# Performance work log

Measured on AMD Instinct MI355X. Metric: run time of the kernel, lower is better.

Reference implementation:

```python
import jax, jax.numpy as jnp
import numpy as np

EPS = 1e-5

def _ln(x, g, b):
    m = jnp.mean(x, axis=-1, keepdims=True)
    v = jnp.var(x, axis=-1, keepdims=True)
    return (x - m) * jax.lax.rsqrt(v + EPS) * g + b

def _gelu(x):
    return jax.nn.gelu(x, approximate=False)  # torch nn.GELU default is exact erf

def setup_inputs() -> dict:
    key = jax.random.key(0)
    B, N, D, H = 4, 1024, 128, 12
    HID = H * D
    ks = jax.random.split(key, 16)
    s = lambda k, sh, fan: jax.random.normal(k, sh, jnp.float32) * (fan ** -0.5)
    return {
        "x": jax.random.normal(ks[0], (B, N, D), jnp.float32),
        # project: LN(D) -> Linear(D,HID) -> GELU -> Linear(HID,HID)
        "ln1_g": jnp.ones((D,), jnp.float32), "ln1_b": jnp.zeros((D,), jnp.float32),
        "W1": s(ks[1], (D, HID), D), "b1": jnp.zeros((HID,), jnp.float32),
        "W2": s(ks[2], (HID, HID), HID), "b2": jnp.zeros((HID,), jnp.float32),
        # shared Attention(inc=D, outc=D)
        "aln_g": jnp.ones((D,), jnp.float32), "aln_b": jnp.zeros((D,), jnp.float32),
        "Wqkv": s(ks[3], (D, 3 * D), D), "bqkv": jnp.zeros((3 * D,), jnp.float32),
        "Wl": s(ks[4], (D, D), D), "bl": jnp.zeros((D,), jnp.float32),
        # out_proj: LN(HID) -> Linear(HID, D) -> GELU
        "lno_g": jnp.ones((HID,), jnp.float32), "lno_b": jnp.zeros((HID,), jnp.float32),
        "Wo": s(ks[5], (HID, D), HID), "bo": jnp.zeros((D,), jnp.float32),
    }

def reference(x, ln1_g, ln1_b, W1, b1, W2, b2,
              aln_g, aln_b, Wqkv, bqkv, Wl, bl,
              lno_g, lno_b, Wo, bo):
    B, N, D = x.shape
    # project (dropout is identity in eval mode)
    h = _ln(x, ln1_g, ln1_b)
    h = _gelu(h @ W1 + b1)
    h = h @ W2 + b2                      # [B, N, H*D]
    H = h.shape[-1] // D
    # chunk along last dim into H features of width D; fold heads into batch
    f = h.reshape(B, N, H, D).transpose(0, 2, 1, 3).reshape(B * H, N, D)
    # shared Attention applied to each head-chunk
    a = _ln(f, aln_g, aln_b)
    qkv = a @ Wqkv + bqkv
    q, k, v = jnp.split(qkv, 3, axis=-1)
    scores = jax.nn.softmax(jnp.einsum('bnd,bmd->bnm', q, k) * (D ** -0.5), axis=-1)
    o = jnp.einsum('bnm,bmd->bnd', scores, v)
    o = o @ Wl + bl
    o = _gelu(o + f)                     # [B*H, N, D]
    # concat heads back along last dim
    feats = o.reshape(B, H, N, D).transpose(0, 2, 1, 3).reshape(B, N, H * D)
    out = _gelu(_ln(feats, lno_g, lno_b) @ Wo + bo)
    return out
```

## Files before the change

kernel.cpp:

```cpp
#include <hip/hip_runtime.h>
#include <stdint.h>

typedef unsigned short u16;
typedef __attribute__((ext_vector_type(8))) short short8;
typedef __attribute__((ext_vector_type(4))) float floatx4;

__device__ inline float b2f(u16 u) {
  union { uint32_t i; float f; } x; x.i = ((uint32_t)u) << 16; return x.f;
}
__device__ inline u16 f2b(float f) {
  union { float f; uint32_t i; } x; x.f = f;
  uint32_t r = (x.i + 0x7FFFu + ((x.i >> 16) & 1u)) >> 16;
  return (u16)r;
}
__device__ inline float gelu_f(float v) {
  return 0.5f * v * (1.0f + erff(v * 0.70710678118654752440f));
}

#define MFMA16(a, b, c) __builtin_amdgcn_mfma_f32_16x16x32_bf16((a), (b), (c), 0, 0, 0)

__device__ __forceinline__ void gl2lds16(const u16* g, u16* l) {
  __builtin_amdgcn_global_load_lds(
      (const __attribute__((address_space(1))) uint32_t*)(uintptr_t)g,
      (__attribute__((address_space(3))) uint32_t*)(uint32_t)(uintptr_t)l,
      16, 0, 0);
}

__global__ __launch_bounds__(256)
void tpose_all_kernel(const float* __restrict__ W1, const float* __restrict__ W2,
                      const float* __restrict__ Wqkv, const float* __restrict__ Wl,
                      const float* __restrict__ Wo,
                      u16* __restrict__ w1t, u16* __restrict__ w2t,
                      u16* __restrict__ wqkvt, u16* __restrict__ wlt,
                      u16* __restrict__ wot) {
  int id = blockIdx.x;
  const float* src; u16* dst; int R, C, bx, by;
  if (id < 2304)      { src = W2;   dst = w2t;   R = 1536; C = 1536; bx = (id % 48) * 32; by = (id / 48) * 32; }
  else if (id < 2496) { id -= 2304; src = W1;   dst = w1t;   R = 128;  C = 1536; bx = (id % 48) * 32; by = (id / 48) * 32; }
  else if (id < 2688) { id -= 2496; src = Wo;   dst = wot;   R = 1536; C = 128;  bx = (id % 4) * 32;  by = (id / 4) * 32; }
  else if (id < 2736) { id -= 2688; src = Wqkv; dst = wqkvt; R = 128;  C = 384;  bx = (id % 12) * 32; by = (id / 12) * 32; }
  else                { id -= 2736; src = Wl;   dst = wlt;   R = 128;  C = 128;  bx = (id % 4) * 32;  by = (id / 4) * 32; }
  __shared__ u16 t[32][33];
  int tx = threadIdx.x & 31, ty = threadIdx.x >> 5;
  for (int i = 0; i < 32; i += 8)
    t[ty + i][tx] = f2b(src[(size_t)(by + ty + i) * C + bx + tx]);
  __syncthreads();
  for (int i = 0; i < 32; i += 8)
    dst[(size_t)(bx + ty + i) * R + by + tx] = t[tx][ty + i];
}

__global__ __launch_bounds__(256)
void vtrans_kernel(const u16* __restrict__ qkv, u16* __restrict__ vT) {
  int bh = blockIdx.y;
  int n0 = blockIdx.x * 32;
  int b = bh / 12, h = bh % 12;
  const int rs = 12 * 384;
  const u16* vp = qkv + (((size_t)b * 1024) * 12 + h) * 384 + 256;
  __shared__ u16 t[4][32][33];
  int tx = threadIdx.x & 31, ty = threadIdx.x >> 5;
  for (int dt = 0; dt < 4; dt++)
    for (int i = 0; i < 32; i += 8)
      t[dt][ty + i][tx] = vp[(size_t)(n0 + ty + i) * rs + dt * 32 + tx];
  __syncthreads();
  u16* dp = vT + (size_t)bh * 128 * 1024 + n0;
  for (int dt = 0; dt < 4; dt++)
    for (int i = 0; i < 32; i += 8)
      dp[(size_t)(dt * 32 + ty + i) * 1024 + tx] = t[dt][tx][ty + i];
}

__global__ __launch_bounds__(256)
void ln128_f32_kernel(const float* __restrict__ X, const float* __restrict__ g,
                      const float* __restrict__ bb, u16* __restrict__ Y) {
  int tid = threadIdx.x, w = tid >> 6, lane = tid & 63;
  int row = blockIdx.x * 4 + w;
  const float* xr = X + (size_t)row * 128;
  float2 xv = *(const float2*)(xr + lane * 2);
  float x0 = xv.x, x1 = xv.y;
  float s = x0 + x1, s2 = x0 * x0 + x1 * x1;
  for (int m = 1; m < 64; m <<= 1) { s += __shfl_xor(s, m, 64); s2 += __shfl_xor(s2, m, 64); }
  float mean = s * (1.0f / 128.0f);
  float var = s2 * (1.0f / 128.0f) - mean * mean;
  float rstd = 1.0f / sqrtf(var + 1e-5f);
  float2 gv = *(const float2*)(g + lane * 2);
  float2 bv = *(const float2*)(bb + lane * 2);
  float y0 = (x0 - mean) * rstd * gv.x + bv.x;
  float y1 = (x1 - mean) * rstd * gv.y + bv.y;
  *(uint32_t*)(Y + (size_t)row * 128 + lane * 2) =
      (uint32_t)f2b(y0) | ((uint32_t)f2b(y1) << 16);
}

__global__ __launch_bounds__(256)
void ln128_bf16_kernel(const u16* __restrict__ X, const float* __restrict__ g,
                       const float* __restrict__ bb, u16* __restrict__ Y) {
  int tid = threadIdx.x, w = tid >> 6, lane = tid & 63;
  int row = blockIdx.x * 4 + w;
  const u16* xr = X + (size_t)row * 128;
  uint32_t u = *(const uint32_t*)(xr + lane * 2);
  float x0 = b2f(u & 0xffff), x1 = b2f(u >> 16);
  float s = x0 + x1, s2 = x0 * x0 + x1 * x1;
  for (int m = 1; m < 64; m <<= 1) { s += __shfl_xor(s, m, 64); s2 += __shfl_xor(s2, m, 64); }
  float mean = s * (1.0f / 128.0f);
  float var = s2 * (1.0f / 128.0f) - mean * mean;
  float rstd = 1.0f / sqrtf(var + 1e-5f);
  float2 gv = *(const float2*)(g + lane * 2);
  float2 bv = *(const float2*)(bb + lane * 2);
  float y0 = (x0 - mean) * rstd * gv.x + bv.x;
  float y1 = (x1 - mean) * rstd * gv.y + bv.y;
  *(uint32_t*)(Y + (size_t)row * 128 + lane * 2) =
      (uint32_t)f2b(y0) | ((uint32_t)f2b(y1) << 16);
}

__global__ __launch_bounds__(256)
void ln1536_kernel(const u16* __restrict__ X, const float* __restrict__ g,
                   const float* __restrict__ bb, u16* __restrict__ Y) {
  int row = blockIdx.x, tid = threadIdx.x;
  const u16* xr = X + (size_t)row * 1536;
  uint32_t u0 = *(const uint32_t*)(xr + tid * 6);
  uint32_t u1 = *(const uint32_t*)(xr + tid * 6 + 2);
  uint32_t u2 = *(const uint32_t*)(xr + tid * 6 + 4);
  float v[6] = { b2f(u0 & 0xffff), b2f(u0 >> 16), b2f(u1 & 0xffff),
                 b2f(u1 >> 16),    b2f(u2 & 0xffff), b2f(u2 >> 16) };
  float s = 0.f, s2 = 0.f;
  for (int j = 0; j < 6; j++) { s += v[j]; s2 += v[j] * v[j]; }
  for (int m = 1; m < 64; m <<= 1) { s += __shfl_xor(s, m, 64); s2 += __shfl_xor(s2, m, 64); }
  __shared__ float red[8];
  int w = tid >> 6, lane = tid & 63;
  if (lane == 0) { red[w] = s; red[4 + w] = s2; }
  __syncthreads();
  s = red[0] + red[1] + red[2] + red[3];
  s2 = red[4] + red[5] + red[6] + red[7];
  float mean = s * (1.0f / 1536.0f);
  float var = s2 * (1.0f / 1536.0f) - mean * mean;
  float rstd = 1.0f / sqrtf(var + 1e-5f);
  uint32_t o[3];
  for (int p = 0; p < 3; p++) {
    int c = tid * 6 + p * 2;
    float y0 = (v[p * 2] - mean) * rstd * g[c] + bb[c];
    float y1 = (v[p * 2 + 1] - mean) * rstd * g[c + 1] + bb[c + 1];
    o[p] = (uint32_t)f2b(y0) | ((uint32_t)f2b(y1) << 16);
  }
  u16* yr = Y + (size_t)row * 1536 + tid * 6;
  *(uint32_t*)(yr) = o[0];
  *(uint32_t*)(yr + 2) = o[1];
  *(uint32_t*)(yr + 4) = o[2];
}

template <int GELU, int RES, typename OUTT>
__global__ __launch_bounds__(256)
void gemm_kernel(const u16* __restrict__ A, const u16* __restrict__ BT,
                 const float* __restrict__ bias, const u16* __restrict__ res,
                 OUTT* __restrict__ C, int M, int N, int K) {
  __shared__ __align__(16) u16 abuf[128 * 32];
  __shared__ __align__(16) u16 bbuf[128 * 32];
  int tid = threadIdx.x;
  int w = tid >> 6, lane = tid & 63, ln = lane & 15, quad = lane >> 4;
  int bm = blockIdx.x * 128, bn = blockIdx.y * 128;
  int wr = w >> 1, wc = w & 1;
  floatx4 acc[4][4] = {};
  for (int k0 = 0; k0 < K; k0 += 32) {
    __syncthreads();
    for (int rd = 0; rd < 2; rd++) {
      int c = tid + rd * 256;
      int row = c >> 2, col = (c & 3) * 8;
      gl2lds16(A + (size_t)(bm + row) * K + k0 + col, abuf + c * 8);
      gl2lds16(BT + (size_t)(bn + row) * K + k0 + col, bbuf + c * 8);
    }
    __syncthreads();
    short8 af[4], bf[4];
    for (int i = 0; i < 4; i++)
      af[i] = *(const short8*)(abuf + (wr * 64 + i * 16 + ln) * 32 + quad * 8);
    for (int j = 0; j < 4; j++)
      bf[j] = *(const short8*)(bbuf + (wc * 64 + j * 16 + ln) * 32 + quad * 8);
    for (int i = 0; i < 4; i++)
      for (int j = 0; j < 4; j++)
        acc[i][j] = MFMA16(af[i], bf[j], acc[i][j]);
  }
  for (int i = 0; i < 4; i++) {
    int row0 = bm + wr * 64 + i * 16 + quad * 4;
    for (int j = 0; j < 4; j++) {
      int col = bn + wc * 64 + j * 16 + ln;
      float bv = bias[col];
      for (int r = 0; r < 4; r++) {
        float v = acc[i][j][r] + bv;
        if (RES) v += b2f(res[(size_t)(row0 + r) * N + col]);
        if (GELU) v = gelu_f(v);
        if constexpr (sizeof(OUTT) == 2)
          C[(size_t)(row0 + r) * N + col] = f2b(v);
        else
          C[(size_t)(row0 + r) * N + col] = v;
      }
    }
  }
}

template <int GELU, int RES, typename OUTT>
__global__ __launch_bounds__(256)
void gemm64_kernel(const u16* __restrict__ A, const u16* __restrict__ BT,
                   const float* __restrict__ bias, const u16* __restrict__ res,
                   OUTT* __restrict__ C, int M, int N, int K) {
  __shared__ __align__(16) u16 abuf[64 * 32];
  __shared__ __align__(16) u16 bbuf[128 * 32];
  int tid = threadIdx.x;
  int w = tid >> 6, lane = tid & 63, ln = lane & 15, quad = lane >> 4;
  int bm = blockIdx.x * 64, bn = blockIdx.y * 128;
  floatx4 acc[4][2] = {};
  for (int k0 = 0; k0 < K; k0 += 32) {
    __syncthreads();
    for (int rd = 0; rd < 2; rd++) {
      int c = tid + rd * 256;
      int row = c >> 2, col = (c & 3) * 8;
      gl2lds16(BT + (size_t)(bn + row) * K + k0 + col, bbuf + c * 8);
    }
    {
      int c = tid;
      int row = c >> 2, col = (c & 3) * 8;
      gl2lds16(A + (size_t)(bm + row) * K + k0 + col, abuf + c * 8);
    }
    __syncthreads();
    short8 af[4], bf[2];
    for (int i = 0; i < 4; i++)
      af[i] = *(const short8*)(abuf + (i * 16 + ln) * 32 + quad * 8);
    for (int j = 0; j < 2; j++)
      bf[j] = *(const short8*)(bbuf + (w * 32 + j * 16 + ln) * 32 + quad * 8);
    for (int i = 0; i < 4; i++)
      for (int j = 0; j < 2; j++)
        acc[i][j] = MFMA16(af[i], bf[j], acc[i][j]);
  }
  for (int i = 0; i < 4; i++) {
    int row0 = bm + i * 16 + quad * 4;
    for (int j = 0; j < 2; j++) {
      int col = bn + w * 32 + j * 16 + ln;
      float bv = bias[col];
      for (int r = 0; r < 4; r++) {
        float v = acc[i][j][r] + bv;
        if (RES) v += b2f(res[(size_t)(row0 + r) * N + col]);
        if (GELU) v = gelu_f(v);
        if constexpr (sizeof(OUTT) == 2)
          C[(size_t)(row0 + r) * N + col] = f2b(v);
        else
          C[(size_t)(row0 + r) * N + col] = v;
      }
    }
  }
}

template <int GELU, int RES, typename OUTT>
__global__ __launch_bounds__(256)
void gemm64b_kernel(const u16* __restrict__ A, const u16* __restrict__ BT,
                    const float* __restrict__ bias, const u16* __restrict__ res,
                    OUTT* __restrict__ C, int M, int N, int K) {
  __shared__ __align__(16) u16 abuf[2 * 64 * 32];
  __shared__ __align__(16) u16 bbuf[2 * 128 * 32];
  int tid = threadIdx.x;
  int w = tid >> 6, lane = tid & 63, ln = lane & 15, quad = lane >> 4;
  int bm = blockIdx.x * 64, bn = blockIdx.y * 128;
  floatx4 acc[4][2] = {};
  for (int k0 = 0; k0 < K; k0 += 64) {
    __syncthreads();
    for (int ks = 0; ks < 2; ks++) {
      {
        int c = tid;
        int row = c >> 2, cc = c & 3;
        gl2lds16(A + (size_t)(bm + row) * K + k0 + ks * 32 + cc * 8,
                 abuf + ks * 2048 + c * 8);
      }
      for (int rd = 0; rd < 2; rd++) {
        int c = tid + rd * 256;
        int row = c >> 2, cc = c & 3;
        gl2lds16(BT + (size_t)(bn + row) * K + k0 + ks * 32 + cc * 8,
                 bbuf + ks * 4096 + c * 8);
      }
    }
    __syncthreads();
    short8 af[2][4], bf[2][2];
    for (int ks = 0; ks < 2; ks++) {
      for (int i = 0; i < 4; i++)
        af[ks][i] = *(const short8*)(abuf + ks * 2048 + (i * 16 + ln) * 32 + quad * 8);
      for (int j = 0; j < 2; j++)
        bf[ks][j] = *(const short8*)(bbuf + ks * 4096 + (w * 32 + j * 16 + ln) * 32 + quad * 8);
    }
    for (int i = 0; i < 4; i++)
      for (int j = 0; j < 2; j++) {
        acc[i][j] = MFMA16(af[0][i], bf[0][j], acc[i][j]);
        acc[i][j] = MFMA16(af[1][i], bf[1][j], acc[i][j]);
      }
  }
  for (int i = 0; i < 4; i++) {
    int row0 = bm + i * 16 + quad * 4;
    for (int j = 0; j < 2; j++) {
      int col = bn + w * 32 + j * 16 + ln;
      float bv = bias[col];
      for (int r = 0; r < 4; r++) {
        float v = acc[i][j][r] + bv;
        if (RES) v += b2f(res[(size_t)(row0 + r) * N + col]);
        if (GELU) v = gelu_f(v);
        if constexpr (sizeof(OUTT) == 2)
          C[(size_t)(row0 + r) * N + col] = f2b(v);
        else
          C[(size_t)(row0 + r) * N + col] = v;
      }
    }
  }
}

__global__ __launch_bounds__(256)
void gemm64_part_kernel(const u16* __restrict__ A, const u16* __restrict__ BT,
                        float* __restrict__ pws, int Kfull, int kspan) {
  __shared__ __align__(16) u16 abuf[64 * 32];
  __shared__ __align__(16) u16 bbuf[128 * 32];
  int tid = threadIdx.x;
  int w = tid >> 6, lane = tid & 63, ln = lane & 15, quad = lane >> 4;
  int bm = blockIdx.x * 64;
  int kbeg = blockIdx.y * kspan, kend = kbeg + kspan;
  float* Cp = pws + (size_t)blockIdx.y * 4096 * 128;
  floatx4 acc[4][2] = {};
  for (int k0 = kbeg; k0 < kend; k0 += 32) {
    __syncthreads();
    for (int rd = 0; rd < 2; rd++) {
      int c = tid + rd * 256;
      int row = c >> 2, col = (c & 3) * 8;
      gl2lds16(BT + (size_t)row * Kfull + k0 + col, bbuf + c * 8);
    }
    {
      int c = tid;
      int row = c >> 2, col = (c & 3) * 8;
      gl2lds16(A + (size_t)(bm + row) * Kfull + k0 + col, abuf + c * 8);
    }
    __syncthreads();
    short8 af[4], bf[2];
    for (int i = 0; i < 4; i++)
      af[i] = *(const short8*)(abuf + (i * 16 + ln) * 32 + quad * 8);
    for (int j = 0; j < 2; j++)
      bf[j] = *(const short8*)(bbuf + (w * 32 + j * 16 + ln) * 32 + quad * 8);
    for (int i = 0; i < 4; i++)
      for (int j = 0; j < 2; j++)
        acc[i][j] = MFMA16(af[i], bf[j], acc[i][j]);
  }
  for (int i = 0; i < 4; i++) {
    int row0 = bm + i * 16 + quad * 4;
    for (int j = 0; j < 2; j++) {
      int col = w * 32 + j * 16 + ln;
      for (int r = 0; r < 4; r++)
        Cp[(size_t)(row0 + r) * 128 + col] = acc[i][j][r];
    }
  }
}

__global__ __launch_bounds__(256)
void combine_wo_kernel(const float* __restrict__ p, const float* __restrict__ bias,
                       float* __restrict__ out) {
  int i = blockIdx.x * 256 + threadIdx.x;
  const int SZ = 4096 * 128;
  float v = p[i] + p[i + SZ] + p[i + 2 * SZ] + p[i + 3 * SZ] + bias[i & 127];
  out[i] = gelu_f(v);
}

__global__ __launch_bounds__(256)
void attn_kernel(const u16* __restrict__ qkv, const u16* __restrict__ vT,
                 u16* __restrict__ obuf) {
  int blk = blockIdx.x;
  int xcd = blk & 7, slot = blk >> 3;
  int bh = xcd * 6 + (slot >> 4);
  int qt = slot & 15;
  int b = bh / 12, hh = bh % 12;
  int tid = threadIdx.x, w = tid >> 6, lane = tid & 63, ln = lane & 15, quad = lane >> 4;
  __shared__ __align__(16) u16 kbuf[4 * 64 * 32];
  __shared__ __align__(16) u16 vbuf[2 * 128 * 32];
  __shared__ __align__(16) u16 pbuf[4][16 * 72];
  const int rs = 12 * 384;
  size_t base = (((size_t)b * 1024) * 12 + hh) * 384;
  const u16* qp = qkv + base;
  const u16* kp = qkv + base + 128;
  const u16* vp = vT + (size_t)bh * 128 * 1024;

  short8 onesb;
  {
    short v = (ln == 0) ? (short)0x3F80 : (short)0;
    for (int j = 0; j < 8; j++) onesb[j] = v;
  }

  int qrow = qt * 64 + w * 16 + ln;
  short8 qf[4];
  for (int st = 0; st < 4; st++)
    qf[st] = *(const short8*)(qp + (size_t)qrow * rs + st * 32 + quad * 8);

  floatx4 o[9] = {};
  const float K2 = 0.08838834764831845f * 1.4426950408889634f;

  for (int kt = 0; kt < 16; kt++) {
    __syncthreads();
    for (int it = 0; it < 4; it++) {
      int c = it * 256 + tid;
      int st = c >> 8, key = (c >> 2) & 63, cc = c & 3;
      gl2lds16(kp + (size_t)(kt * 64 + key) * rs + st * 32 + cc * 8, kbuf + c * 8);
      int kf = c >> 9, d = (c >> 2) & 127;
      gl2lds16(vp + (size_t)d * 1024 + kt * 64 + kf * 32 + cc * 8, vbuf + c * 8);
    }
    __syncthreads();

    floatx4 s[4] = {};
    for (int t = 0; t < 4; t++)
      for (int st = 0; st < 4; st++) {
        short8 bk = *(const short8*)(kbuf + st * 2048 + (t * 16 + ln) * 32 + quad * 8);
        s[t] = MFMA16(qf[st], bk, s[t]);
      }
    for (int r = 0; r < 4; r++) {
      int prow = (quad * 4 + r) * 72;
      pbuf[w][prow + ln]      = f2b(exp2f(s[0][r] * K2));
      pbuf[w][prow + 16 + ln] = f2b(exp2f(s[1][r] * K2));
      pbuf[w][prow + 32 + ln] = f2b(exp2f(s[2][r] * K2));
      pbuf[w][prow + 48 + ln] = f2b(exp2f(s[3][r] * K2));
    }
    for (int kf = 0; kf < 2; kf++) {
      short8 ap = *(const short8*)(&pbuf[w][ln * 72 + kf * 32 + quad * 8]);
      for (int dt = 0; dt < 8; dt++) {
        short8 bv = *(const short8*)(vbuf + kf * 4096 + (dt * 16 + ln) * 32 + quad * 8);
        o[dt] = MFMA16(ap, bv, o[dt]);
      }
      o[8] = MFMA16(ap, onesb, o[8]);
    }
  }

  for (int r = 0; r < 4; r++) {
    float l = __shfl(o[8][r], lane & 48);
    float inv = 1.0f / l;
    int n = qt * 64 + w * 16 + quad * 4 + r;
    size_t ob = ((((size_t)b * 1024 + n) * 12) + hh) * 128;
    for (int dt = 0; dt < 8; dt++)
      obuf[ob + dt * 16 + ln] = f2b(o[dt][r] * inv);
  }
}

extern "C" void kernel_launch(void* const* d_in, const int* in_sizes, int n_in,
                              void* d_out, int out_size, void* d_ws, size_t ws_size,
                              hipStream_t stream) {
  (void)in_sizes; (void)n_in; (void)out_size; (void)ws_size;
  const float* x    = (const float*)d_in[0];
  const float* ln1g = (const float*)d_in[1];
  const float* ln1b = (const float*)d_in[2];
  const float* W1   = (const float*)d_in[3];
  const float* b1   = (const float*)d_in[4];
  const float* W2   = (const float*)d_in[5];
  const float* b2   = (const float*)d_in[6];
  const float* alng = (const float*)d_in[7];
  const float* alnb = (const float*)d_in[8];
  const float* Wqkv = (const float*)d_in[9];
  const float* bqkv = (const float*)d_in[10];
  const float* Wl   = (const float*)d_in[11];
  const float* bl   = (const float*)d_in[12];
  const float* lnog = (const float*)d_in[13];
  const float* lnob = (const float*)d_in[14];
  const float* Wo   = (const float*)d_in[15];
  const float* bo   = (const float*)d_in[16];
  float* out = (float*)d_out;

  char* ws = (char*)d_ws;
  size_t off = 0;
  auto alloc = [&](size_t elems) { u16* p = (u16*)(ws + off); off += elems * sizeof(u16); return p; };
  u16* w1t   = alloc((size_t)1536 * 128);
  u16* w2t   = alloc((size_t)1536 * 1536);
  u16* wqkvt = alloc((size_t)384 * 128);
  u16* wlt   = alloc((size_t)128 * 128);
  u16* wot   = alloc((size_t)128 * 1536);
  u16* lnx   = alloc((size_t)4096 * 128);
  u16* h1    = alloc((size_t)4096 * 1536);
  u16* h2    = alloc((size_t)4096 * 1536);
  u16* aln   = alloc((size_t)49152 * 128);
  u16* qkv   = alloc((size_t)49152 * 384);
  u16* obuf = h1;
  u16* vT = aln;
  u16* feats = aln;
  u16* lnf = qkv;
  float* pws = (float*)h1;

  dim3 T(256);
  tpose_all_kernel<<<dim3(2752), T, 0, stream>>>(W1, W2, Wqkv, Wl, Wo,
                                                 w1t, w2t, wqkvt, wlt, wot);
  ln128_f32_kernel<<<dim3(4096 / 4), T, 0, stream>>>(x, ln1g, ln1b, lnx);
  gemm64_kernel<1, 0, u16><<<dim3(4096 / 64, 1536 / 128), T, 0, stream>>>(
      lnx, w1t, b1, nullptr, h1, 4096, 1536, 128);
  gemm64b_kernel<0, 0, u16><<<dim3(4096 / 64, 1536 / 128), T, 0, stream>>>(
      h1, w2t, b2, nullptr, h2, 4096, 1536, 1536);
  ln128_bf16_kernel<<<dim3(49152 / 4), T, 0, stream>>>(h2, alng, alnb, aln);
  gemm_kernel<0, 0, u16><<<dim3(49152 / 128, 384 / 128), T, 0, stream>>>(
      aln, wqkvt, bqkv, nullptr, qkv, 49152, 384, 128);
  vtrans_kernel<<<dim3(1024 / 32, 48), T, 0, stream>>>(qkv, vT);
  attn_kernel<<<dim3(768), T, 0, stream>>>(qkv, vT, obuf);
  gemm64_kernel<1, 1, u16><<<dim3(49152 / 64, 1), T, 0, stream>>>(
      obuf, wlt, bl, h2, feats, 49152, 128, 128);
  ln1536_kernel<<<dim3(4096), T, 0, stream>>>(feats, lnog, lnob, lnf);
  gemm64_part_kernel<<<dim3(4096 / 64, 4), T, 0, stream>>>(lnf, wot, pws, 1536, 384);
  combine_wo_kernel<<<dim3(4096 * 128 / 256), T, 0, stream>>>(pws, bo, out);
}
```

Baseline: 261.7 us.

## Fuse LayerNorm(128) into the following GEMM prologues for W1 and QKV

Removes the standalone ln128 kernels and computes LayerNorm inside a new gemmln kernel. Each block normalizes its 64 input rows into padded LDS and then streams only the weight tiles. This drops two launches and the round trip of the normalized activations through global memory, most notably the 49152x128 aln buffer. In exchange the LN is recomputed by every column block (3 for QKV, 12 for W1), and the QKV GEMM moves from 128x128 to 64x128 tiles.

```diff
diff --git a/kernel.cpp b/kernel.cpp
--- a/kernel.cpp
+++ b/kernel.cpp
@@ -66,48 +66,6 @@
   for (int dt = 0; dt < 4; dt++)
     for (int i = 0; i < 32; i += 8)
       dp[(size_t)(dt * 32 + ty + i) * 1024 + tx] = t[dt][tx][ty + i];
-}
-
-__global__ __launch_bounds__(256)
-void ln128_f32_kernel(const float* __restrict__ X, const float* __restrict__ g,
-                      const float* __restrict__ bb, u16* __restrict__ Y) {
-  int tid = threadIdx.x, w = tid >> 6, lane = tid & 63;
-  int row = blockIdx.x * 4 + w;
-  const float* xr = X + (size_t)row * 128;
-  float2 xv = *(const float2*)(xr + lane * 2);
-  float x0 = xv.x, x1 = xv.y;
-  float s = x0 + x1, s2 = x0 * x0 + x1 * x1;
-  for (int m = 1; m < 64; m <<= 1) { s += __shfl_xor(s, m, 64); s2 += __shfl_xor(s2, m, 64); }
-  float mean = s * (1.0f / 128.0f);
-  float var = s2 * (1.0f / 128.0f) - mean * mean;
-  float rstd = 1.0f / sqrtf(var + 1e-5f);
-  float2 gv = *(const float2*)(g + lane * 2);
-  float2 bv = *(const float2*)(bb + lane * 2);
-  float y0 = (x0 - mean) * rstd * gv.x + bv.x;
-  float y1 = (x1 - mean) * rstd * gv.y + bv.y;
-  *(uint32_t*)(Y + (size_t)row * 128 + lane * 2) =
-      (uint32_t)f2b(y0) | ((uint32_t)f2b(y1) << 16);
-}
-
-__global__ __launch_bounds__(256)
-void ln128_bf16_kernel(const u16* __restrict__ X, const float* __restrict__ g,
-                       const float* __restrict__ bb, u16* __restrict__ Y) {
-  int tid = threadIdx.x, w = tid >> 6, lane = tid & 63;
-  int row = blockIdx.x * 4 + w;
-  const u16* xr = X + (size_t)row * 128;
-  uint32_t u = *(const uint32_t*)(xr + lane * 2);
-  float x0 = b2f(u & 0xffff), x1 = b2f(u >> 16);
-  float s = x0 + x1, s2 = x0 * x0 + x1 * x1;
-  for (int m = 1; m < 64; m <<= 1) { s += __shfl_xor(s, m, 64); s2 += __shfl_xor(s2, m, 64); }
-  float mean = s * (1.0f / 128.0f);
-  float var = s2 * (1.0f / 128.0f) - mean * mean;
-  float rstd = 1.0f / sqrtf(var + 1e-5f);
-  float2 gv = *(const float2*)(g + lane * 2);
-  float2 bv = *(const float2*)(bb + lane * 2);
-  float y0 = (x0 - mean) * rstd * gv.x + bv.x;
-  float y1 = (x1 - mean) * rstd * gv.y + bv.y;
-  *(uint32_t*)(Y + (size_t)row * 128 + lane * 2) =
-      (uint32_t)f2b(y0) | ((uint32_t)f2b(y1) << 16);
 }
 
 __global__ __launch_bounds__(256)
@@ -145,49 +103,77 @@
   *(uint32_t*)(yr + 4) = o[2];
 }
 
-template <int GELU, int RES, typename OUTT>
-__global__ __launch_bounds__(256)
-void gemm_kernel(const u16* __restrict__ A, const u16* __restrict__ BT,
-                 const float* __restrict__ bias, const u16* __restrict__ res,
-                 OUTT* __restrict__ C, int M, int N, int K) {
-  __shared__ __align__(16) u16 abuf[128 * 32];
+template <int SRCF32, int GELU>
+__global__ __launch_bounds__(256)
+void gemmln_kernel(const void* __restrict__ Xv, const float* __restrict__ lng,
+                   const float* __restrict__ lnb, const u16* __restrict__ BT,
+                   const float* __restrict__ bias, u16* __restrict__ C, int N) {
+  __shared__ __align__(16) u16 abuf[64 * 136];
   __shared__ __align__(16) u16 bbuf[128 * 32];
   int tid = threadIdx.x;
   int w = tid >> 6, lane = tid & 63, ln = lane & 15, quad = lane >> 4;
-  int bm = blockIdx.x * 128, bn = blockIdx.y * 128;
-  int wr = w >> 1, wc = w & 1;
-  floatx4 acc[4][4] = {};
-  for (int k0 = 0; k0 < K; k0 += 32) {
+  int bm = blockIdx.x * 64, bn = blockIdx.y * 128;
+  {
+    int row = tid >> 2, part = tid & 3;
+    float xv[32];
+    if (SRCF32) {
+      const float* xr = (const float*)Xv + (size_t)(bm + row) * 128 + part * 32;
+      for (int j = 0; j < 8; j++) {
+        float4 v = *(const float4*)(xr + j * 4);
+        xv[j * 4 + 0] = v.x; xv[j * 4 + 1] = v.y;
+        xv[j * 4 + 2] = v.z; xv[j * 4 + 3] = v.w;
+      }
+    } else {
+      const u16* xr = (const u16*)Xv + (size_t)(bm + row) * 128 + part * 32;
+      for (int j = 0; j < 4; j++) {
+        uint4 v = *(const uint4*)(xr + j * 8);
+        const u16* pp = (const u16*)&v;
+        for (int e = 0; e < 8; e++) xv[j * 8 + e] = b2f(pp[e]);
+      }
+    }
+    float s = 0.f, s2 = 0.f;
+    for (int j = 0; j < 32; j++) { s += xv[j]; s2 += xv[j] * xv[j]; }
+    s += __shfl_xor(s, 1, 64);  s2 += __shfl_xor(s2, 1, 64);
+    s += __shfl_xor(s, 2, 64);  s2 += __shfl_xor(s2, 2, 64);
+    float mean = s * (1.0f / 128.0f);
+    float var = s2 * (1.0f / 128.0f) - mean * mean;
+    float rstd = 1.0f / sqrtf(var + 1e-5f);
+    for (int j = 0; j < 32; j += 8) {
+      u16 tmp[8];
+      for (int e = 0; e < 8; e++) {
+        int cc = part * 32 + j + e;
+        tmp[e] = f2b((xv[j + e] - mean) * rstd * lng[cc] + lnb[cc]);
+      }
+      *(uint4*)(abuf + row * 136 + part * 32 + j) = *(const uint4*)tmp;
+    }
+  }
+  floatx4 acc[4][2] = {};
+  for (int k0 = 0; k0 < 128; k0 += 32) {
     __syncthreads();
     for (int rd = 0; rd < 2; rd++) {
       int c = tid + rd * 256;
       int row = c >> 2, col = (c & 3) * 8;
-      gl2lds16(A + (size_t)(bm + row) * K + k0 + col, abuf + c * 8);
-      gl2lds16(BT + (size_t)(bn + row) * K + k0 + col, bbuf + c * 8);
-    }
-    __syncthreads();
-    short8 af[4], bf[4];
-    for (int i = 0; i < 4; i++)
-      af[i] = *(const short8*)(abuf + (wr * 64 + i * 16 + ln) * 32 + quad * 8);
-    for (int j = 0; j < 4; j++)
-      bf[j] = *(const short8*)(bbuf + (wc * 64 + j * 16 + ln) * 32 + quad * 8);
-    for (int i = 0; i < 4; i++)
-      for (int j = 0; j < 4; j++)
+      gl2lds16(BT + (size_t)(bn + row) * 128 + k0 + col, bbuf + c * 8);
+    }
+    __syncthreads();
+    short8 af[4], bf[2];
+    for (int i = 0; i < 4; i++)
+      af[i] = *(const short8*)(abuf + (i * 16 + ln) * 136 + k0 + quad * 8);
+    for (int j = 0; j < 2; j++)
+      bf[j] = *(const short8*)(bbuf + (w * 32 + j * 16 + ln) * 32 + quad * 8);
+    for (int i = 0; i < 4; i++)
+      for (int j = 0; j < 2; j++)
         acc[i][j] = MFMA16(af[i], bf[j], acc[i][j]);
   }
   for (int i = 0; i < 4; i++) {
-    int row0 = bm + wr * 64 + i * 16 + quad * 4;
-    for (int j = 0; j < 4; j++) {
-      int col = bn + wc * 64 + j * 16 + ln;
+    int row0 = bm + i * 16 + quad * 4;
+    for (int j = 0; j < 2; j++) {
+      int col = bn + w * 32 + j * 16 + ln;
       float bv = bias[col];
       for (int r = 0; r < 4; r++) {
         float v = acc[i][j][r] + bv;
-        if (RES) v += b2f(res[(size_t)(row0 + r) * N + col]);
         if (GELU) v = gelu_f(v);
-        if constexpr (sizeof(OUTT) == 2)
-          C[(size_t)(row0 + r) * N + col] = f2b(v);
-        else
-          C[(size_t)(row0 + r) * N + col] = v;
+        C[(size_t)(row0 + r) * N + col] = f2b(v);
       }
     }
   }
@@ -462,7 +448,6 @@
   u16* wqkvt = alloc((size_t)384 * 128);
   u16* wlt   = alloc((size_t)128 * 128);
   u16* wot   = alloc((size_t)128 * 1536);
-  u16* lnx   = alloc((size_t)4096 * 128);
   u16* h1    = alloc((size_t)4096 * 1536);
   u16* h2    = alloc((size_t)4096 * 1536);
   u16* aln   = alloc((size_t)49152 * 128);
@@ -476,14 +461,12 @@
   dim3 T(256);
   tpose_all_kernel<<<dim3(2752), T, 0, stream>>>(W1, W2, Wqkv, Wl, Wo,
                                                  w1t, w2t, wqkvt, wlt, wot);
-  ln128_f32_kernel<<<dim3(4096 / 4), T, 0, stream>>>(x, ln1g, ln1b, lnx);
-  gemm64_kernel<1, 0, u16><<<dim3(4096 / 64, 1536 / 128), T, 0, stream>>>(
-      lnx, w1t, b1, nullptr, h1, 4096, 1536, 128);
+  gemmln_kernel<1, 1><<<dim3(4096 / 64, 1536 / 128), T, 0, stream>>>(
+      x, ln1g, ln1b, w1t, b1, h1, 1536);
   gemm64b_kernel<0, 0, u16><<<dim3(4096 / 64, 1536 / 128), T, 0, stream>>>(
       h1, w2t, b2, nullptr, h2, 4096, 1536, 1536);
-  ln128_bf16_kernel<<<dim3(49152 / 4), T, 0, stream>>>(h2, alng, alnb, aln);
-  gemm_kernel<0, 0, u16><<<dim3(49152 / 128, 384 / 128), T, 0, stream>>>(
-      aln, wqkvt, bqkv, nullptr, qkv, 49152, 384, 128);
+  gemmln_kernel<0, 0><<<dim3(49152 / 64, 384 / 128), T, 0, stream>>>(
+      h2, alng, alnb, wqkvt, bqkv, qkv, 384);
   vtrans_kernel<<<dim3(1024 / 32, 48), T, 0, stream>>>(qkv, vT);
   attn_kernel<<<dim3(768), T, 0, stream>>>(qkv, vT, obuf);
   gemm64_kernel<1, 1, u16><<<dim3(49152 / 64, 1), T, 0, stream>>>(
```

Result: slower. 268.8 us (+2.7%).

## Switch attention kernel to 32x32 MFMA with split-key warps and LDS merge

Applied to the files above, without the earlier changes.

The attention kernel moves from 16x16x32 to 32x32x16 bf16 MFMA tiles. Each wave now handles 32 query rows over half of every 64-key tile, with two waves sharing a query slab. The K, V and P LDS layouts are reshaped to match the new operand fragments. At the end the two key-halves' partial outputs and row sums are merged through LDS. The intent is fewer MFMA and LDS read instructions per FLOP, at the cost of an extra reduction phase, a barrier and more accumulator registers.

```diff
diff --git a/kernel.cpp b/kernel.cpp
--- a/kernel.cpp
+++ b/kernel.cpp
@@ -4,6 +4,7 @@
 typedef unsigned short u16;
 typedef __attribute__((ext_vector_type(8))) short short8;
 typedef __attribute__((ext_vector_type(4))) float floatx4;
+typedef __attribute__((ext_vector_type(16))) float floatx16;
 
 __device__ inline float b2f(u16 u) {
   union { uint32_t i; float f; } x; x.i = ((uint32_t)u) << 16; return x.f;
@@ -18,6 +19,7 @@
 }
 
 #define MFMA16(a, b, c) __builtin_amdgcn_mfma_f32_16x16x32_bf16((a), (b), (c), 0, 0, 0)
+#define MFMA32(a, b, c) __builtin_amdgcn_mfma_f32_32x32x16_bf16((a), (b), (c), 0, 0, 0)
 
 __device__ __forceinline__ void gl2lds16(const u16* g, u16* l) {
   __builtin_amdgcn_global_load_lds(
@@ -363,10 +365,12 @@
   int bh = xcd * 6 + (slot >> 4);
   int qt = slot & 15;
   int b = bh / 12, hh = bh % 12;
-  int tid = threadIdx.x, w = tid >> 6, lane = tid & 63, ln = lane & 15, quad = lane >> 4;
-  __shared__ __align__(16) u16 kbuf[4 * 64 * 32];
-  __shared__ __align__(16) u16 vbuf[2 * 128 * 32];
-  __shared__ __align__(16) u16 pbuf[4][16 * 72];
+  int tid = threadIdx.x, w = tid >> 6, lane = tid & 63;
+  int col = lane & 31, half = lane >> 5;
+  int qs = w >> 1, kh = w & 1;
+  __shared__ __align__(16) u16 kbuf[16 * 64 * 8];
+  __shared__ __align__(16) u16 vbuf[8 * 128 * 8];
+  __shared__ __align__(16) u16 pbuf[4][32 * 40];
   const int rs = 12 * 384;
   size_t base = (((size_t)b * 1024) * 12 + hh) * 384;
   const u16* qp = qkv + base;
@@ -375,59 +379,80 @@
 
   short8 onesb;
   {
-    short v = (ln == 0) ? (short)0x3F80 : (short)0;
+    short v = (col == 0) ? (short)0x3F80 : (short)0;
     for (int j = 0; j < 8; j++) onesb[j] = v;
   }
 
-  int qrow = qt * 64 + w * 16 + ln;
-  short8 qf[4];
-  for (int st = 0; st < 4; st++)
-    qf[st] = *(const short8*)(qp + (size_t)qrow * rs + st * 32 + quad * 8);
-
-  floatx4 o[9] = {};
+  int qrow = qt * 64 + qs * 32 + col;
+  short8 qf[8];
+  for (int kk = 0; kk < 8; kk++)
+    qf[kk] = *(const short8*)(qp + (size_t)qrow * rs + kk * 16 + half * 8);
+
+  floatx16 o[4] = {};
+  floatx16 ol = {};
   const float K2 = 0.08838834764831845f * 1.4426950408889634f;
 
   for (int kt = 0; kt < 16; kt++) {
     __syncthreads();
     for (int it = 0; it < 4; it++) {
       int c = it * 256 + tid;
-      int st = c >> 8, key = (c >> 2) & 63, cc = c & 3;
-      gl2lds16(kp + (size_t)(kt * 64 + key) * rs + st * 32 + cc * 8, kbuf + c * 8);
-      int kf = c >> 9, d = (c >> 2) & 127;
-      gl2lds16(vp + (size_t)d * 1024 + kt * 64 + kf * 32 + cc * 8, vbuf + c * 8);
-    }
-    __syncthreads();
-
-    floatx4 s[4] = {};
-    for (int t = 0; t < 4; t++)
-      for (int st = 0; st < 4; st++) {
-        short8 bk = *(const short8*)(kbuf + st * 2048 + (t * 16 + ln) * 32 + quad * 8);
-        s[t] = MFMA16(qf[st], bk, s[t]);
-      }
-    for (int r = 0; r < 4; r++) {
-      int prow = (quad * 4 + r) * 72;
-      pbuf[w][prow + ln]      = f2b(exp2f(s[0][r] * K2));
-      pbuf[w][prow + 16 + ln] = f2b(exp2f(s[1][r] * K2));
-      pbuf[w][prow + 32 + ln] = f2b(exp2f(s[2][r] * K2));
-      pbuf[w][prow + 48 + ln] = f2b(exp2f(s[3][r] * K2));
-    }
-    for (int kf = 0; kf < 2; kf++) {
-      short8 ap = *(const short8*)(&pbuf[w][ln * 72 + kf * 32 + quad * 8]);
-      for (int dt = 0; dt < 8; dt++) {
-        short8 bv = *(const short8*)(vbuf + kf * 4096 + (dt * 16 + ln) * 32 + quad * 8);
-        o[dt] = MFMA16(ap, bv, o[dt]);
-      }
-      o[8] = MFMA16(ap, onesb, o[8]);
-    }
-  }
-
-  for (int r = 0; r < 4; r++) {
-    float l = __shfl(o[8][r], lane & 48);
-    float inv = 1.0f / l;
-    int n = qt * 64 + w * 16 + quad * 4 + r;
-    size_t ob = ((((size_t)b * 1024 + n) * 12) + hh) * 128;
-    for (int dt = 0; dt < 8; dt++)
-      obuf[ob + dt * 16 + ln] = f2b(o[dt][r] * inv);
+      int kc = c >> 6, key = c & 63;
+      gl2lds16(kp + (size_t)(kt * 64 + key) * rs + kc * 8, kbuf + c * 8);
+      int vc = c >> 7, d = c & 127;
+      gl2lds16(vp + (size_t)d * 1024 + kt * 64 + vc * 8, vbuf + c * 8);
+    }
+    __syncthreads();
+
+    floatx16 s = {};
+    for (int kk = 0; kk < 8; kk++) {
+      short8 bk = *(const short8*)(kbuf + (kk * 2 + half) * 512 + (kh * 32 + col) * 8);
+      s = MFMA32(qf[kk], bk, s);
+    }
+    for (int r = 0; r < 16; r++) {
+      int q = (r & 3) + 8 * (r >> 2) + 4 * half;
+      pbuf[w][q * 40 + col] = f2b(exp2f(s[r] * K2));
+    }
+    short8 pf[2];
+    for (int ks = 0; ks < 2; ks++)
+      pf[ks] = *(const short8*)(pbuf[w] + col * 40 + ks * 16 + half * 8);
+    for (int ks = 0; ks < 2; ks++) {
+      int kc = kh * 4 + ks * 2 + half;
+      for (int dt = 0; dt < 4; dt++) {
+        short8 bv = *(const short8*)(vbuf + kc * 1024 + (dt * 32 + col) * 8);
+        o[dt] = MFMA32(pf[ks], bv, o[dt]);
+      }
+      ol = MFMA32(pf[ks], onesb, ol);
+    }
+  }
+
+  __syncthreads();
+  float* mbuf = (float*)(qs == 0 ? (void*)kbuf : (void*)vbuf);
+  if (kh == 1) {
+    for (int dt = 0; dt < 4; dt++)
+      for (int r = 0; r < 16; r++)
+        mbuf[(dt * 16 + r) * 64 + lane] = o[dt][r];
+    if (col == 0) {
+      float* lb = (float*)&pbuf[w][0];
+      for (int r = 0; r < 16; r++) {
+        int q = (r & 3) + 8 * (r >> 2) + 4 * half;
+        lb[q] = ol[r];
+      }
+    }
+  }
+  __syncthreads();
+  if (kh == 0) {
+    const float* lb = (const float*)&pbuf[w + 1][0];
+    for (int r = 0; r < 16; r++) {
+      int q = (r & 3) + 8 * (r >> 2) + 4 * half;
+      float lown = __shfl(ol[r], lane & 32);
+      float inv = 1.0f / (lown + lb[q]);
+      int n = qt * 64 + qs * 32 + q;
+      size_t ob = ((((size_t)b * 1024 + n) * 12) + hh) * 128;
+      for (int dt = 0; dt < 4; dt++) {
+        float val = (o[dt][r] + mbuf[(dt * 16 + r) * 64 + lane]) * inv;
+        obuf[ob + dt * 32 + col] = f2b(val);
+      }
+    }
   }
 }
 
```

Measured after the change: 296.3 us. +13.2%, slower.

## Switch attention intermediates to head-major layout and fuse V transpose into QKV GEMM

Applied to the files above, without the earlier changes.

The attention-side LayerNorm now reads h2 with a head permutation and writes rows in (b,h,n) order. The QKV GEMM writes Q/K compactly with a 256-wide row stride and writes V directly in transposed form, which removes the separate vtrans kernel. The attention output is stored head-major, and a new Wl GEMM scatters its GELU+residual result back into the token-major feats layout. This cuts one kernel launch and a full read/write pass over V, at the cost of strided 8-byte V stores and scattered stores in the Wl epilogue.

```diff
diff --git a/kernel.cpp b/kernel.cpp
--- a/kernel.cpp
+++ b/kernel.cpp
@@ -50,25 +50,6 @@
 }
 
 __global__ __launch_bounds__(256)
-void vtrans_kernel(const u16* __restrict__ qkv, u16* __restrict__ vT) {
-  int bh = blockIdx.y;
-  int n0 = blockIdx.x * 32;
-  int b = bh / 12, h = bh % 12;
-  const int rs = 12 * 384;
-  const u16* vp = qkv + (((size_t)b * 1024) * 12 + h) * 384 + 256;
-  __shared__ u16 t[4][32][33];
-  int tx = threadIdx.x & 31, ty = threadIdx.x >> 5;
-  for (int dt = 0; dt < 4; dt++)
-    for (int i = 0; i < 32; i += 8)
-      t[dt][ty + i][tx] = vp[(size_t)(n0 + ty + i) * rs + dt * 32 + tx];
-  __syncthreads();
-  u16* dp = vT + (size_t)bh * 128 * 1024 + n0;
-  for (int dt = 0; dt < 4; dt++)
-    for (int i = 0; i < 32; i += 8)
-      dp[(size_t)(dt * 32 + ty + i) * 1024 + tx] = t[dt][tx][ty + i];
-}
-
-__global__ __launch_bounds__(256)
 void ln128_f32_kernel(const float* __restrict__ X, const float* __restrict__ g,
                       const float* __restrict__ bb, u16* __restrict__ Y) {
   int tid = threadIdx.x, w = tid >> 6, lane = tid & 63;
@@ -90,11 +71,13 @@
 }
 
 __global__ __launch_bounds__(256)
-void ln128_bf16_kernel(const u16* __restrict__ X, const float* __restrict__ g,
+void ln128_perm_kernel(const u16* __restrict__ X, const float* __restrict__ g,
                        const float* __restrict__ bb, u16* __restrict__ Y) {
   int tid = threadIdx.x, w = tid >> 6, lane = tid & 63;
-  int row = blockIdx.x * 4 + w;
-  const u16* xr = X + (size_t)row * 128;
+  int rid = blockIdx.x * 4 + w;
+  int bh = rid >> 10, n = rid & 1023;
+  int b = bh / 12, h = bh % 12;
+  const u16* xr = X + ((size_t)(b * 1024 + n)) * 1536 + h * 128;
   uint32_t u = *(const uint32_t*)(xr + lane * 2);
   float x0 = b2f(u & 0xffff), x1 = b2f(u >> 16);
   float s = x0 + x1, s2 = x0 * x0 + x1 * x1;
@@ -106,7 +89,7 @@
   float2 bv = *(const float2*)(bb + lane * 2);
   float y0 = (x0 - mean) * rstd * gv.x + bv.x;
   float y1 = (x1 - mean) * rstd * gv.y + bv.y;
-  *(uint32_t*)(Y + (size_t)row * 128 + lane * 2) =
+  *(uint32_t*)(Y + (size_t)rid * 128 + lane * 2) =
       (uint32_t)f2b(y0) | ((uint32_t)f2b(y1) << 16);
 }
 
@@ -145,11 +128,11 @@
   *(uint32_t*)(yr + 4) = o[2];
 }
 
-template <int GELU, int RES, typename OUTT>
-__global__ __launch_bounds__(256)
-void gemm_kernel(const u16* __restrict__ A, const u16* __restrict__ BT,
-                 const float* __restrict__ bias, const u16* __restrict__ res,
-                 OUTT* __restrict__ C, int M, int N, int K) {
+__global__ __launch_bounds__(256)
+void qkv_kernel(const u16* __restrict__ A, const u16* __restrict__ BT,
+                const float* __restrict__ bias, u16* __restrict__ qkv,
+                u16* __restrict__ vT) {
+  const int K = 128;
   __shared__ __align__(16) u16 abuf[128 * 32];
   __shared__ __align__(16) u16 bbuf[128 * 32];
   int tid = threadIdx.x;
@@ -175,19 +158,28 @@
       for (int j = 0; j < 4; j++)
         acc[i][j] = MFMA16(af[i], bf[j], acc[i][j]);
   }
-  for (int i = 0; i < 4; i++) {
-    int row0 = bm + wr * 64 + i * 16 + quad * 4;
-    for (int j = 0; j < 4; j++) {
-      int col = bn + wc * 64 + j * 16 + ln;
-      float bv = bias[col];
-      for (int r = 0; r < 4; r++) {
-        float v = acc[i][j][r] + bv;
-        if (RES) v += b2f(res[(size_t)(row0 + r) * N + col]);
-        if (GELU) v = gelu_f(v);
-        if constexpr (sizeof(OUTT) == 2)
-          C[(size_t)(row0 + r) * N + col] = f2b(v);
-        else
-          C[(size_t)(row0 + r) * N + col] = v;
+  if (blockIdx.y < 2) {
+    for (int i = 0; i < 4; i++) {
+      int row0 = bm + wr * 64 + i * 16 + quad * 4;
+      for (int j = 0; j < 4; j++) {
+        int col = bn + wc * 64 + j * 16 + ln;
+        float bv = bias[col];
+        for (int r = 0; r < 4; r++)
+          qkv[(size_t)(row0 + r) * 256 + col] = f2b(acc[i][j][r] + bv);
+      }
+    }
+  } else {
+    int bh = bm >> 10;
+    int nb = bm & 1023;
+    u16* vp = vT + (size_t)bh * 128 * 1024;
+    for (int i = 0; i < 4; i++) {
+      int n0 = nb + wr * 64 + i * 16 + quad * 4;
+      for (int j = 0; j < 4; j++) {
+        int d = wc * 64 + j * 16 + ln;
+        float bv = bias[256 + d];
+        u16 tmp[4];
+        for (int r = 0; r < 4; r++) tmp[r] = f2b(acc[i][j][r] + bv);
+        *(uint2*)(vp + (size_t)d * 1024 + n0) = *(const uint2*)tmp;
       }
     }
   }
@@ -304,6 +296,56 @@
 }
 
 __global__ __launch_bounds__(256)
+void gemmwl_kernel(const u16* __restrict__ A, const u16* __restrict__ BT,
+                   const float* __restrict__ bias, const u16* __restrict__ res,
+                   u16* __restrict__ feats) {
+  const int K = 128;
+  __shared__ __align__(16) u16 abuf[64 * 32];
+  __shared__ __align__(16) u16 bbuf[128 * 32];
+  int tid = threadIdx.x;
+  int w = tid >> 6, lane = tid & 63, ln = lane & 15, quad = lane >> 4;
+  int bm = blockIdx.x * 64;
+  floatx4 acc[4][2] = {};
+  for (int k0 = 0; k0 < K; k0 += 32) {
+    __syncthreads();
+    for (int rd = 0; rd < 2; rd++) {
+      int c = tid + rd * 256;
+      int row = c >> 2, col = (c & 3) * 8;
+      gl2lds16(BT + (size_t)row * K + k0 + col, bbuf + c * 8);
+    }
+    {
+      int c = tid;
+      int row = c >> 2, col = (c & 3) * 8;
+      gl2lds16(A + (size_t)(bm + row) * K + k0 + col, abuf + c * 8);
+    }
+    __syncthreads();
+    short8 af[4], bf[2];
+    for (int i = 0; i < 4; i++)
+      af[i] = *(const short8*)(abuf + (i * 16 + ln) * 32 + quad * 8);
+    for (int j = 0; j < 2; j++)
+      bf[j] = *(const short8*)(bbuf + (w * 32 + j * 16 + ln) * 32 + quad * 8);
+    for (int i = 0; i < 4; i++)
+      for (int j = 0; j < 2; j++)
+        acc[i][j] = MFMA16(af[i], bf[j], acc[i][j]);
+  }
+  int bh = bm >> 10, nb = bm & 1023;
+  int b = bh / 12, hh = bh % 12;
+  size_t obase = ((size_t)b * 1024) * 1536 + hh * 128;
+  for (int i = 0; i < 4; i++) {
+    int n0 = nb + i * 16 + quad * 4;
+    for (int j = 0; j < 2; j++) {
+      int col = w * 32 + j * 16 + ln;
+      float bv = bias[col];
+      for (int r = 0; r < 4; r++) {
+        size_t idx = obase + (size_t)(n0 + r) * 1536 + col;
+        float v = acc[i][j][r] + bv + b2f(res[idx]);
+        feats[idx] = f2b(gelu_f(v));
+      }
+    }
+  }
+}
+
+__global__ __launch_bounds__(256)
 void gemm64_part_kernel(const u16* __restrict__ A, const u16* __restrict__ BT,
                         float* __restrict__ pws, int Kfull, int kspan) {
   __shared__ __align__(16) u16 abuf[64 * 32];
@@ -362,13 +404,12 @@
   int xcd = blk & 7, slot = blk >> 3;
   int bh = xcd * 6 + (slot >> 4);
   int qt = slot & 15;
-  int b = bh / 12, hh = bh % 12;
   int tid = threadIdx.x, w = tid >> 6, lane = tid & 63, ln = lane & 15, quad = lane >> 4;
   __shared__ __align__(16) u16 kbuf[4 * 64 * 32];
   __shared__ __align__(16) u16 vbuf[2 * 128 * 32];
   __shared__ __align__(16) u16 pbuf[4][16 * 72];
-  const int rs = 12 * 384;
-  size_t base = (((size_t)b * 1024) * 12 + hh) * 384;
+  const int rs = 256;
+  size_t base = (size_t)bh * 1024 * 256;
   const u16* qp = qkv + base;
   const u16* kp = qkv + base + 128;
   const u16* vp = vT + (size_t)bh * 128 * 1024;
@@ -425,7 +466,7 @@
     float l = __shfl(o[8][r], lane & 48);
     float inv = 1.0f / l;
     int n = qt * 64 + w * 16 + quad * 4 + r;
-    size_t ob = ((((size_t)b * 1024 + n) * 12) + hh) * 128;
+    size_t ob = ((size_t)bh * 1024 + n) * 128;
     for (int dt = 0; dt < 8; dt++)
       obuf[ob + dt * 16 + ln] = f2b(o[dt][r] * inv);
   }
@@ -466,9 +507,9 @@
   u16* h1    = alloc((size_t)4096 * 1536);
   u16* h2    = alloc((size_t)4096 * 1536);
   u16* aln   = alloc((size_t)49152 * 128);
-  u16* qkv   = alloc((size_t)49152 * 384);
-  u16* obuf = h1;
-  u16* vT = aln;
+  u16* qkv   = alloc((size_t)49152 * 256);
+  u16* obuf  = alloc((size_t)49152 * 128);
+  u16* vT = h1;
   u16* feats = aln;
   u16* lnf = qkv;
   float* pws = (float*)h1;
@@ -481,13 +522,10 @@
       lnx, w1t, b1, nullptr, h1, 4096, 1536, 128);
   gemm64b_kernel<0, 0, u16><<<dim3(4096 / 64, 1536 / 128), T, 0, stream>>>(
       h1, w2t, b2, nullptr, h2, 4096, 1536, 1536);
-  ln128_bf16_kernel<<<dim3(49152 / 4), T, 0, stream>>>(h2, alng, alnb, aln);
-  gemm_kernel<0, 0, u16><<<dim3(49152 / 128, 384 / 128), T, 0, stream>>>(
-      aln, wqkvt, bqkv, nullptr, qkv, 49152, 384, 128);
-  vtrans_kernel<<<dim3(1024 / 32, 48), T, 0, stream>>>(qkv, vT);
+  ln128_perm_kernel<<<dim3(49152 / 4), T, 0, stream>>>(h2, alng, alnb, aln);
+  qkv_kernel<<<dim3(49152 / 128, 3), T, 0, stream>>>(aln, wqkvt, bqkv, qkv, vT);
   attn_kernel<<<dim3(768), T, 0, stream>>>(qkv, vT, obuf);
-  gemm64_kernel<1, 1, u16><<<dim3(49152 / 64, 1), T, 0, stream>>>(
-      obuf, wlt, bl, h2, feats, 49152, 128, 128);
+  gemmwl_kernel<<<dim3(49152 / 64), T, 0, stream>>>(obuf, wlt, bl, h2, feats);
   ln1536_kernel<<<dim3(4096), T, 0, stream>>>(feats, lnog, lnob, lnf);
   gemm64_part_kernel<<<dim3(4096 / 64, 4), T, 0, stream>>>(lnf, wot, pws, 1536, 384);
   combine_wo_kernel<<<dim3(4096 * 128 / 256), T, 0, stream>>>(pws, bo, out);
```

Measured after the change: 254.0 us. -2.9%, faster.
